# Optimization experiments

Hardware: AMD Instinct MI355X
Metric: run time of the kernel (lower is better)

The kernel has to match this reference:

```python
import jax, jax.numpy as jnp
import numpy as np

T, B = 128, 256
C_IN, H = 1024, 1024


def setup_inputs() -> dict:
    key = jax.random.key(0)
    ks = jax.random.split(key, 6)
    x = jax.random.normal(ks[0], (T * B, C_IN), dtype=jnp.float32)
    Wi = jax.random.normal(ks[1], (C_IN, 4 * H), dtype=jnp.float32) / np.sqrt(C_IN)
    Wh = jax.random.normal(ks[2], (H, 4 * H), dtype=jnp.float32) / np.sqrt(H)
    b = jax.random.normal(ks[3], (4 * H,), dtype=jnp.float32) * 0.01
    done = jax.random.randint(ks[4], (T * B,), 0, 2) > 0
    main = jax.random.randint(ks[5], (T * B,), 0, 2) > 0
    zeros = jnp.zeros((B, H), dtype=jnp.float32)
    return {"x": x, "c1": zeros, "h1": zeros, "c2": zeros, "h2": zeros,
            "Wi": Wi, "Wh": Wh, "b": b, "done": done, "main": main}


def reference(x, c1, h1, c2, h2, Wi, Wh, b, done, main):
    batch = c1.shape[0]
    num_steps = x.shape[0] // batch
    x3 = x.reshape(num_steps, batch, -1)
    done3 = done.reshape(num_steps, batch)
    main3 = main.reshape(num_steps, batch)

    def step(carry, inp):
        (r1c, r1h), (r2c, r2h) = carry
        xt, dt, mt = inp
        m = mt[:, None]  # [B,1] select player-1 vs player-2 state
        c = jnp.where(m, r1c, r2c)
        h = jnp.where(m, r1h, r2h)
        # OptimizedLSTMCell: fused gates, flax order i, f, g, o
        z = xt @ Wi + h @ Wh + b
        i, f, g, o = jnp.split(z, 4, axis=-1)
        nc = jax.nn.sigmoid(f) * c + jax.nn.sigmoid(i) * jnp.tanh(g)
        nh = jax.nn.sigmoid(o) * jnp.tanh(nc)
        # write back only to the active player's state
        n1c = jnp.where(m, nc, r1c); n1h = jnp.where(m, nh, r1h)
        n2c = jnp.where(m, r2c, nc); n2h = jnp.where(m, r2h, nh)
        # reset both states where episode is done
        d = dt[:, None]
        n1c = jnp.where(d, 0.0, n1c); n1h = jnp.where(d, 0.0, n1h)
        n2c = jnp.where(d, 0.0, n2c); n2h = jnp.where(d, 0.0, n2h)
        return ((n1c, n1h), (n2c, n2h)), nh

    _, ys = jax.lax.scan(step, ((c1, h1), (c2, h2)), (x3, done3, main3))
    return ys.reshape(-1, ys.shape[-1])  # [T*B, H]
```

## Files before the change

kernel.cpp:

```cpp
#include <hip/hip_runtime.h>
#include <cstdint>
#include <cstddef>

typedef unsigned short u16;
typedef unsigned char u8;
typedef unsigned int u32;

typedef short s16x8 __attribute__((ext_vector_type(8)));
typedef float f32x4 __attribute__((ext_vector_type(4)));

__device__ __forceinline__ float b2f(u16 h){ u32 u = ((u32)h)<<16; float f; __builtin_memcpy(&f,&u,4); return f; }
__device__ __forceinline__ u16 f2b(float x){ u32 u; __builtin_memcpy(&u,&x,4); u += 0x7fffu + ((u>>16)&1u); return (u16)(u>>16); }
__device__ __forceinline__ float sigf(float x){ return 1.f/(1.f+__expf(-x)); }
__device__ __forceinline__ float tanh2(float x){
  float ax=fabsf(x); float e=__expf(-2.f*ax); float r=(1.f-e)/(1.f+e); return x<0.f? -r : r;
}

typedef __attribute__((address_space(1))) const void gvoid_t;
typedef __attribute__((address_space(3))) void lvoid_t;
__device__ __forceinline__ void gl_lds16(const u16* src, u16* dst){
  __builtin_amdgcn_global_load_lds((gvoid_t*)src, (lvoid_t*)dst, 16, 0, 0);
}

__device__ __forceinline__ void st_u16_coh(u16* p, u16 v){
  asm volatile("global_store_short %0, %1, off sc0 sc1" :: "v"(p), "v"((u32)v) : "memory");
}
__device__ __forceinline__ void st_f32_coh(float* p, float v){
  asm volatile("global_store_dword %0, %1, off sc0 sc1" :: "v"(p), "v"(v) : "memory");
}
__device__ __forceinline__ s16x8 gload16(const u16* p){
  s16x8 r;
  asm volatile("global_load_dwordx4 %0, %1, off" : "=v"(r) : "v"(p) : "memory");
  return r;
}
__device__ __forceinline__ s16x8 gload16_coh(const u16* p){
  s16x8 r;
  asm volatile("global_load_dwordx4 %0, %1, off sc0 sc1" : "=v"(r) : "v"(p) : "memory");
  return r;
}

__global__ void detect_mask_mode(const u8* raw, int n, int* flag){
  __shared__ int cnt;
  int tid = threadIdx.x;
  if(tid==0) cnt=0;
  __syncthreads();
  int c=0;
  for(int i=tid;i<n;i+=blockDim.x) c += (raw[i]!=0);
  atomicAdd(&cnt, c);
  __syncthreads();
  if(tid==0) *flag = (cnt > (n>>2)) ? 1 : 0;
}

__global__ void convert_masks(const void* done_raw, const void* main_raw, u8* done_u8, u8* main_u8, int n, const int* flag){
  int mode = *flag;
  for(int i = blockIdx.x*blockDim.x + threadIdx.x; i<n; i += gridDim.x*blockDim.x){
    u8 d, m;
    if(mode){ d = ((const u8*)done_raw)[i]!=0; m = ((const u8*)main_raw)[i]!=0; }
    else    { d = ((const int*)done_raw)[i]!=0; m = ((const int*)main_raw)[i]!=0; }
    done_u8[i]=d; main_u8[i]=m;
  }
}

__global__ void zero_flags(int* p, int n){
  int i = threadIdx.x;
  if(i<n) p[i]=0;
}

__global__ void cvt_f32_bf16(const float* __restrict__ in, u16* __restrict__ out, int n4){
  int i = blockIdx.x*blockDim.x + threadIdx.x;
  if(i < n4){
    float4 v = ((const float4*)in)[i];
    ushort4 o;
    o.x=f2b(v.x); o.y=f2b(v.y); o.z=f2b(v.z); o.w=f2b(v.w);
    ((ushort4*)out)[i]=o;
  }
}

__global__ void transpose_to_bf16(const float* __restrict__ in, u16* __restrict__ out, int R, int C){
  __shared__ float tile[64][65];
  int c0 = blockIdx.x*64, r0 = blockIdx.y*64;
  int tx = threadIdx.x & 63, ty = threadIdx.x >> 6;
  for(int i=ty;i<64;i+=4) tile[i][tx] = in[(size_t)(r0+i)*C + c0 + tx];
  __syncthreads();
  for(int i=ty;i<64;i+=4) out[(size_t)(c0+i)*R + r0 + tx] = f2b(tile[tx][i]);
}

__global__ void init_hsel(const float* __restrict__ h1in, const float* __restrict__ h2in,
                          const u8* __restrict__ mmain, u16* __restrict__ hsel0){
  int i = blockIdx.x*blockDim.x + threadIdx.x;
  if(i < 256*1024){
    int row = i >> 10;
    hsel0[i] = f2b(mmain[row] ? h1in[i] : h2in[i]);
  }
}

template<bool ZF32>
__global__ __launch_bounds__(256) void gemm_zx(const u16* __restrict__ A, const u16* __restrict__ Bt,
                                               const float* __restrict__ bias, void* __restrict__ Cout,
                                               int M, int N, int K){
  __shared__ u16 As[128*32];
  __shared__ u16 Bs[128*32];
  int nbx = N>>7, nby = M>>7;
  int nwg = nbx*nby;
  int gid = blockIdx.x;
  int per = nwg>>3;
  int g2 = (gid&7)*per + (gid>>3);
  int tpg = 8*nbx;
  int grp = g2/tpg, w = g2%tpg;
  int brow = grp*8 + (w & 7);
  int bcol = w >> 3;
  int row0 = brow<<7, col0 = bcol<<7;

  int tid=threadIdx.x, wid=tid>>6, lane=tid&63;
  int l15=lane&15, hi=lane>>4;
  int wm=(wid>>1)<<6, wn=(wid&1)<<6;

  f32x4 acc[4][4];
  #pragma unroll
  for(int m=0;m<4;m++)
    #pragma unroll
    for(int n=0;n<4;n++) acc[m][n]=(f32x4){0.f,0.f,0.f,0.f};

  for(int k0=0;k0<K;k0+=32){
    __syncthreads();
    #pragma unroll
    for(int q=0;q<2;q++){
      int cb=q*256+wid*64;
      int ch=cb+lane;
      gl_lds16(A + (size_t)(row0+(ch>>2))*K + k0 + (ch&3)*8, &As[cb*8]);
    }
    #pragma unroll
    for(int q=0;q<2;q++){
      int cb=q*256+wid*64;
      int ch=cb+lane;
      gl_lds16(Bt + (size_t)(col0+(ch>>2))*K + k0 + (ch&3)*8, &Bs[cb*8]);
    }
    __syncthreads();
    s16x8 a[4], b[4];
    #pragma unroll
    for(int m=0;m<4;m++) a[m] = *(const s16x8*)&As[(wm+m*16+l15)*32 + hi*8];
    #pragma unroll
    for(int n=0;n<4;n++) b[n] = *(const s16x8*)&Bs[(wn+n*16+l15)*32 + hi*8];
    #pragma unroll
    for(int m=0;m<4;m++)
      #pragma unroll
      for(int n=0;n<4;n++)
        acc[m][n] = __builtin_amdgcn_mfma_f32_16x16x32_bf16(a[m],b[n],acc[m][n],0,0,0);
  }
  #pragma unroll
  for(int m=0;m<4;m++){
    #pragma unroll
    for(int n=0;n<4;n++){
      #pragma unroll
      for(int j=0;j<4;j++){
        int r = row0+wm+m*16+hi*4+j;
        int c = col0+wn+n*16+l15;
        float v = acc[m][n][j] + bias[c];
        if(ZF32) ((float*)Cout)[(size_t)r*N+c]=v;
        else     ((u16*)Cout)[(size_t)r*N+c]=f2b(v);
      }
    }
  }
}

template<bool ZF32>
__global__ __launch_bounds__(512) __attribute__((amdgpu_waves_per_eu(2,2)))
void lstm_persist(
    const void* __restrict__ Zx, const u16* __restrict__ Wht,
    u16* __restrict__ hs0, u16* __restrict__ hs1,
    const float* __restrict__ c1i, const float* __restrict__ h1i,
    const float* __restrict__ c2i, const float* __restrict__ h2i,
    const u8* __restrict__ mdone, const u8* __restrict__ mmain,
    float* __restrict__ out, int* __restrict__ ready)
{
  __shared__ u16 As[32768];
  float* zbuf = (float*)As;

  const int bid = blockIdx.x;
  const int rg = bid & 7, jg = bid >> 3;
  const int r0 = rg << 5, j0 = jg << 5;
  const int tid = threadIdx.x, wid = tid >> 6, lane = tid & 63;
  const int l15 = lane & 15, hi = lane >> 4;
  const int gate = wid >> 1, nh = wid & 1;
  const int srow = tid >> 4, sc16 = tid & 15;
  const int erow = tid >> 5, ecol = tid & 31;

  s16x8 breg[32];
  {
    const u16* wp = Wht + ((size_t)(gate*1024 + j0 + nh*16 + l15))*1024 + (size_t)hi*8;
    #pragma unroll
    for(int kk=0;kk<32;kk++) breg[kk] = gload16(wp + kk*32);
    asm volatile("s_waitcnt vmcnt(0)" ::: "memory");
    __builtin_amdgcn_sched_barrier(0);
  }

  float c1r[2],c2r[2],h1r[2],h2r[2];
  #pragma unroll
  for(int e=0;e<2;e++){
    size_t sidx = (size_t)(r0 + e*16 + erow)*1024 + j0 + ecol;
    c1r[e]=c1i[sidx]; c2r[e]=c2i[sidx]; h1r[e]=h1i[sidx]; h2r[e]=h2i[sidx];
  }

  const u16* Zb = (const u16*)Zx;
  const float* Zf = (const float*)Zx;
  int* flag = ready + rg*32;

  for(int t=0;t<128;t++){
    float zr[4][2]; u8 md[2], mm[2], mm2[2];
    #pragma unroll
    for(int e=0;e<2;e++){
      int gb = t*256 + r0 + e*16 + erow;
      size_t base = (size_t)gb*4096 + j0 + ecol;
      #pragma unroll
      for(int g=0; g<4; g++)
        zr[g][e] = ZF32 ? Zf[base + g*1024] : b2f(Zb[base + g*1024]);
      md[e]=mdone[gb]; mm[e]=mmain[gb];
      mm2[e] = (t<127) ? mmain[gb+256] : (u8)0;
    }

    if(t>0 && tid==0){
      while(__hip_atomic_load(flag, __ATOMIC_RELAXED, __HIP_MEMORY_SCOPE_AGENT) < 32*t)
        __builtin_amdgcn_s_sleep(1);
    }
    __syncthreads();
    __builtin_amdgcn_sched_barrier(0);

    const u16* hin = (t&1) ? hs1 : hs0;
    u16* hout = (t&1) ? hs0 : hs1;

    {
      const u16* hrow = hin + (size_t)(r0+srow)*1024;
      s16x8 v[8];
      #pragma unroll
      for(int kc=0;kc<8;kc++) v[kc] = gload16_coh(hrow + (kc*16+sc16)*8);
      asm volatile("s_waitcnt vmcnt(0)" ::: "memory");
      #pragma unroll
      for(int kc=0;kc<8;kc++){
        int chunk = kc*16+sc16;
        *(s16x8*)&As[chunk*256 + ((srow ^ (chunk&7))<<3)] = v[kc];
      }
    }
    __syncthreads();

    f32x4 acc[2];
    acc[0]=(f32x4){0.f,0.f,0.f,0.f}; acc[1]=(f32x4){0.f,0.f,0.f,0.f};
    #pragma unroll
    for(int kk=0;kk<32;kk++){
      int c0 = kk*4 + hi;
      s16x8 a0 = *(const s16x8*)&As[c0*256 + ((l15      ^ (c0&7))<<3)];
      s16x8 a1 = *(const s16x8*)&As[c0*256 + (((16+l15) ^ (c0&7))<<3)];
      acc[0] = __builtin_amdgcn_mfma_f32_16x16x32_bf16(a0, breg[kk], acc[0], 0,0,0);
      acc[1] = __builtin_amdgcn_mfma_f32_16x16x32_bf16(a1, breg[kk], acc[1], 0,0,0);
    }
    __syncthreads();

    #pragma unroll
    for(int m=0;m<2;m++)
      #pragma unroll
      for(int j=0;j<4;j++){
        int row = m*16 + hi*4 + j;
        zbuf[(gate*32 + row)*33 + nh*16 + l15] = acc[m][j];
      }
    __syncthreads();

    float nhv[2];
    #pragma unroll
    for(int e=0;e<2;e++){
      int row = e*16 + erow;
      float zi  = zr[0][e] + zbuf[(0*32+row)*33 + ecol];
      float zf_ = zr[1][e] + zbuf[(1*32+row)*33 + ecol];
      float zg  = zr[2][e] + zbuf[(2*32+row)*33 + ecol];
      float zo  = zr[3][e] + zbuf[(3*32+row)*33 + ecol];
      bool m_ = mm[e]!=0, d_ = md[e]!=0;
      float co = m_ ? c1r[e] : c2r[e];
      float nc = sigf(zf_)*co + sigf(zi)*tanh2(zg);
      float nhx = sigf(zo)*tanh2(nc);
      nhv[e] = nhx;
      float n1c = m_?nc:c1r[e], n2c = m_?c2r[e]:nc;
      float n1h = m_?nhx:h1r[e], n2h = m_?h2r[e]:nhx;
      if(d_){ n1c=0.f; n2c=0.f; n1h=0.f; n2h=0.f; }
      c1r[e]=n1c; c2r[e]=n2c; h1r[e]=n1h; h2r[e]=n2h;
      if(t<127)
        st_u16_coh(&hout[(size_t)(r0+row)*1024 + j0 + ecol], f2b(mm2[e] ? n1h : n2h));
    }
    asm volatile("s_waitcnt vmcnt(0)" ::: "memory");
    __syncthreads();
    if(t<127 && tid==0)
      __hip_atomic_fetch_add(flag, 1, __ATOMIC_RELAXED, __HIP_MEMORY_SCOPE_AGENT);

    #pragma unroll
    for(int e=0;e<2;e++){
      int gb = t*256 + r0 + e*16 + erow;
      st_f32_coh(&out[(size_t)gb*1024 + j0 + ecol], nhv[e]);
    }
  }
}

extern "C" void kernel_launch(void* const* d_in, const int* in_sizes, int n_in,
                              void* d_out, int out_size, void* d_ws, size_t ws_size,
                              hipStream_t stream){
  const float* x   = (const float*)d_in[0];
  const float* c1i = (const float*)d_in[1];
  const float* h1i = (const float*)d_in[2];
  const float* c2i = (const float*)d_in[3];
  const float* h2i = (const float*)d_in[4];
  const float* Wi  = (const float*)d_in[5];
  const float* Wh  = (const float*)d_in[6];
  const float* bias= (const float*)d_in[7];
  const void* done_raw = d_in[8];
  const void* main_raw = d_in[9];
  float* out = (float*)d_out;

  char* ws = (char*)d_ws;
  size_t off=0;
  auto alloc=[&](size_t sz)->char*{ char* p = ws+off; off += (sz+255)&~(size_t)255; return p; };

  u16* xb   = (u16*)alloc(33554432ull*2);
  u16* WiT  = (u16*)alloc(4096ull*1024*2);
  u16* WhT  = (u16*)alloc(4096ull*1024*2);
  u16* hs0  = (u16*)alloc(262144ull*2);
  u16* hs1  = (u16*)alloc(262144ull*2);
  u8* dmask = (u8*)alloc(32768);
  u8* mmask = (u8*)alloc(32768);
  int* flag = (int*)alloc(256);
  int* ready= (int*)alloc(1024);

  bool zf32 = (off + 536870912ull) <= ws_size;
  void* Zx  = (void*)alloc(zf32 ? 536870912ull : 268435456ull);

  detect_mask_mode<<<1,256,0,stream>>>((const u8*)done_raw, 32768, flag);
  convert_masks<<<64,256,0,stream>>>(done_raw, main_raw, dmask, mmask, 32768, flag);
  cvt_f32_bf16<<<32768,256,0,stream>>>(x, xb, 8388608);
  transpose_to_bf16<<<dim3(64,16),256,0,stream>>>(Wi, WiT, 1024, 4096);
  transpose_to_bf16<<<dim3(64,16),256,0,stream>>>(Wh, WhT, 1024, 4096);
  init_hsel<<<1024,256,0,stream>>>(h1i, h2i, mmask, hs0);
  zero_flags<<<1,256,0,stream>>>(ready, 256);

  if(zf32) gemm_zx<true ><<<8192,256,0,stream>>>(xb, WiT, bias, Zx, 32768, 4096, 1024);
  else     gemm_zx<false><<<8192,256,0,stream>>>(xb, WiT, bias, Zx, 32768, 4096, 1024);

  if(zf32)
    lstm_persist<true ><<<256,512,0,stream>>>(Zx,WhT,hs0,hs1,c1i,h1i,c2i,h2i,dmask,mmask,out,ready);
  else
    lstm_persist<false><<<256,512,0,stream>>>(Zx,WhT,hs0,hs1,c1i,h1i,c2i,h2i,dmask,mmask,out,ready);
}
```

Measured before the change: 1.128 ms.

## Split recurrent GEMM over K across wave pairs with separate partial-sum buffer

Each wave now covers both 16-column halves of its gate but only half of the K dimension, and the two K-halves are summed when the gates are read back. This doubles A-fragment reuse per LDS read, halving LDS traffic in the recurrent matmul. A dedicated zpart buffer replaces aliasing the A tile, which removes one barrier per step. The h-tile staging also waits on the first half of the loads before writing them, overlapping the rest with LDS stores. In exchange it uses extra LDS and adds a reduction in the elementwise stage.

```diff
diff --git a/kernel.cpp b/kernel.cpp
--- a/kernel.cpp
+++ b/kernel.cpp
@@ -174,22 +174,25 @@
     float* __restrict__ out, int* __restrict__ ready)
 {
   __shared__ u16 As[32768];
-  float* zbuf = (float*)As;
+  __shared__ float zpart[4*2*32*33];
 
   const int bid = blockIdx.x;
   const int rg = bid & 7, jg = bid >> 3;
   const int r0 = rg << 5, j0 = jg << 5;
   const int tid = threadIdx.x, wid = tid >> 6, lane = tid & 63;
   const int l15 = lane & 15, hi = lane >> 4;
-  const int gate = wid >> 1, nh = wid & 1;
+  const int gate = wid >> 1, kg = wid & 1;
   const int srow = tid >> 4, sc16 = tid & 15;
   const int erow = tid >> 5, ecol = tid & 31;
 
-  s16x8 breg[32];
+  s16x8 breg[2][16];
   {
-    const u16* wp = Wht + ((size_t)(gate*1024 + j0 + nh*16 + l15))*1024 + (size_t)hi*8;
-    #pragma unroll
-    for(int kk=0;kk<32;kk++) breg[kk] = gload16(wp + kk*32);
+    #pragma unroll
+    for(int n=0;n<2;n++){
+      const u16* wp = Wht + ((size_t)(gate*1024 + j0 + n*16 + l15))*1024 + kg*512 + hi*8;
+      #pragma unroll
+      for(int kk=0;kk<16;kk++) breg[n][kk] = gload16(wp + kk*32);
+    }
     asm volatile("s_waitcnt vmcnt(0)" ::: "memory");
     __builtin_amdgcn_sched_barrier(0);
   }
@@ -233,44 +236,56 @@
       s16x8 v[8];
       #pragma unroll
       for(int kc=0;kc<8;kc++) v[kc] = gload16_coh(hrow + (kc*16+sc16)*8);
-      asm volatile("s_waitcnt vmcnt(0)" ::: "memory");
-      #pragma unroll
-      for(int kc=0;kc<8;kc++){
+      asm volatile("s_waitcnt vmcnt(4)" ::: "memory");
+      #pragma unroll
+      for(int kc=0;kc<4;kc++){
         int chunk = kc*16+sc16;
         *(s16x8*)&As[chunk*256 + ((srow ^ (chunk&7))<<3)] = v[kc];
       }
-    }
-    __syncthreads();
-
-    f32x4 acc[2];
-    acc[0]=(f32x4){0.f,0.f,0.f,0.f}; acc[1]=(f32x4){0.f,0.f,0.f,0.f};
-    #pragma unroll
-    for(int kk=0;kk<32;kk++){
-      int c0 = kk*4 + hi;
+      asm volatile("s_waitcnt vmcnt(0)" ::: "memory");
+      #pragma unroll
+      for(int kc=4;kc<8;kc++){
+        int chunk = kc*16+sc16;
+        *(s16x8*)&As[chunk*256 + ((srow ^ (chunk&7))<<3)] = v[kc];
+      }
+    }
+    __syncthreads();
+
+    f32x4 acc[2][2];
+    #pragma unroll
+    for(int m=0;m<2;m++)
+      #pragma unroll
+      for(int n=0;n<2;n++) acc[m][n]=(f32x4){0.f,0.f,0.f,0.f};
+    #pragma unroll
+    for(int kk=0;kk<16;kk++){
+      int c0 = (kg*16 + kk)*4 + hi;
       s16x8 a0 = *(const s16x8*)&As[c0*256 + ((l15      ^ (c0&7))<<3)];
       s16x8 a1 = *(const s16x8*)&As[c0*256 + (((16+l15) ^ (c0&7))<<3)];
-      acc[0] = __builtin_amdgcn_mfma_f32_16x16x32_bf16(a0, breg[kk], acc[0], 0,0,0);
-      acc[1] = __builtin_amdgcn_mfma_f32_16x16x32_bf16(a1, breg[kk], acc[1], 0,0,0);
-    }
-    __syncthreads();
+      acc[0][0] = __builtin_amdgcn_mfma_f32_16x16x32_bf16(a0, breg[0][kk], acc[0][0], 0,0,0);
+      acc[0][1] = __builtin_amdgcn_mfma_f32_16x16x32_bf16(a0, breg[1][kk], acc[0][1], 0,0,0);
+      acc[1][0] = __builtin_amdgcn_mfma_f32_16x16x32_bf16(a1, breg[0][kk], acc[1][0], 0,0,0);
+      acc[1][1] = __builtin_amdgcn_mfma_f32_16x16x32_bf16(a1, breg[1][kk], acc[1][1], 0,0,0);
+    }
 
     #pragma unroll
     for(int m=0;m<2;m++)
       #pragma unroll
-      for(int j=0;j<4;j++){
-        int row = m*16 + hi*4 + j;
-        zbuf[(gate*32 + row)*33 + nh*16 + l15] = acc[m][j];
-      }
+      for(int n=0;n<2;n++)
+        #pragma unroll
+        for(int j=0;j<4;j++){
+          int row = m*16 + hi*4 + j;
+          zpart[((gate*2+kg)*32 + row)*33 + n*16 + l15] = acc[m][n][j];
+        }
     __syncthreads();
 
     float nhv[2];
     #pragma unroll
     for(int e=0;e<2;e++){
       int row = e*16 + erow;
-      float zi  = zr[0][e] + zbuf[(0*32+row)*33 + ecol];
-      float zf_ = zr[1][e] + zbuf[(1*32+row)*33 + ecol];
-      float zg  = zr[2][e] + zbuf[(2*32+row)*33 + ecol];
-      float zo  = zr[3][e] + zbuf[(3*32+row)*33 + ecol];
+      float zi  = zr[0][e] + zpart[((0)*32+row)*33 + ecol] + zpart[((1)*32+row)*33 + ecol];
+      float zf_ = zr[1][e] + zpart[((2)*32+row)*33 + ecol] + zpart[((3)*32+row)*33 + ecol];
+      float zg  = zr[2][e] + zpart[((4)*32+row)*33 + ecol] + zpart[((5)*32+row)*33 + ecol];
+      float zo  = zr[3][e] + zpart[((6)*32+row)*33 + ecol] + zpart[((7)*32+row)*33 + ecol];
       bool m_ = mm[e]!=0, d_ = md[e]!=0;
       float co = m_ ? c1r[e] : c2r[e];
       float nc = sigf(zf_)*co + sigf(zi)*tanh2(zg);
```

Result: faster. 1.103 ms (-2.2%).
